# Kernel optimization log

Measured on AMD Instinct MI355X. Metric: run time of the kernel, lower is better.

## Reference

```python
import jax, jax.numpy as jnp
import numpy as np

B = 8192       # batch
HID = 1024     # hidden_dim
HEADS = 8      # head_count
OBS, ACT, N_AGENTS = 128, 32, 4
ENC_IN = N_AGENTS * OBS + ACT   # 544
DEC_IN = (N_AGENTS - 1) * ACT   # 96


def _linear(key, fan_in, fan_out):
    k1, k2 = jax.random.split(key)
    lim = 1.0 / np.sqrt(fan_in)
    W = jax.random.uniform(k1, (fan_in, fan_out), minval=-lim, maxval=lim, dtype=jnp.float32)
    b = jax.random.uniform(k2, (fan_out,), minval=-lim, maxval=lim, dtype=jnp.float32)
    return W, b


def setup_inputs() -> dict:
    key = jax.random.key(0)
    ks = jax.random.split(key, 10)
    s = jax.random.normal(ks[0], (B, N_AGENTS * OBS), dtype=jnp.float32)
    a = jax.random.normal(ks[1], (B, N_AGENTS * ACT), dtype=jnp.float32)
    W_enc_in, b_enc_in = _linear(ks[2], ENC_IN, HID)   # encoder_input_fc
    W_dec_in, b_dec_in = _linear(ks[3], DEC_IN, HID)   # decoder_input_fc
    W_eh, b_eh = _linear(ks[4], HID, HID)              # fc_encoder_input
    head_ks = jax.random.split(ks[5], HEADS)
    Wb = [_linear(k, HID, HID) for k in head_ks]       # fc_encoder_heads
    W_heads = jnp.stack([w for w, _ in Wb], axis=0)    # [H, HID, HID]
    b_heads = jnp.stack([b for _, b in Wb], axis=0)    # [H, HID]
    W_dh, b_dh = _linear(ks[6], HID, HID)              # fc_decoder_input
    W1, b1 = _linear(ks[7], HID, HID)                  # fc1
    W2, b2 = _linear(ks[8], HID, 1)                    # fc2
    return {"s": s, "a": a,
            "W_enc_in": W_enc_in, "b_enc_in": b_enc_in,
            "W_dec_in": W_dec_in, "b_dec_in": b_dec_in,
            "W_eh": W_eh, "b_eh": b_eh,
            "W_heads": W_heads, "b_heads": b_heads,
            "W_dh": W_dh, "b_dh": b_dh,
            "W1": W1, "b1": b1, "W2": W2, "b2": b2}


def reference(s, a, W_enc_in, b_enc_in, W_dec_in, b_dec_in, W_eh, b_eh,
              W_heads, b_heads, W_dh, b_dh, W1, b1, W2, b2):
    relu = jax.nn.relu
    # agent id = 0: own action is a[:, :ACT], others' actions are a[:, ACT:]
    enc_input = jnp.concatenate([s, a[:, :ACT]], axis=1) @ W_enc_in + b_enc_in   # [B, HID]
    dec_input = a[:, ACT:] @ W_dec_in + b_dec_in                                 # [B, HID]
    # Attention_ATT_2
    encoder_h = relu(enc_input @ W_eh + b_eh)                                    # [B, HID]
    encoder_heads = relu(jnp.einsum('bd,hde->hbe', encoder_h, W_heads)
                         + b_heads[:, None, :])                                  # [H, B, HID]
    decoder_H = relu(dec_input @ W_dh + b_dh)                                    # [B, HID]
    scores = jnp.einsum('hbd,bd->bh', encoder_heads, decoder_H)                  # [B, H]
    attn = jax.nn.softmax(scores, axis=1)                                        # [B, H]
    context = jnp.einsum('hbd,bh->bd', encoder_heads, attn)                      # [B, HID]
    x = relu(context @ W1 + b1)
    q = x @ W2 + b2                                                              # [B, 1]
    return q
```

## Files before the change

kernel.cpp:

```cpp
#include <hip/hip_runtime.h>
#include <hip/hip_bf16.h>
#include <hip/hip_fp16.h>

#define BATCH   8192
#define HID     1024
#define HEADS   8
#define BC      2048

typedef unsigned int  u32;
typedef unsigned short u16;
typedef __attribute__((ext_vector_type(8))) short bf16x8;
typedef __attribute__((ext_vector_type(4))) float f32x4;

__device__ __forceinline__ u32 pack_hi2(u32 u0, u32 u1) {
    return (u0 >> 16) | (u1 & 0xFFFF0000u);
}
__device__ __forceinline__ void split1(float x, u16& h, u16& l) {
    const u32 u = __float_as_uint(x);
    h = (u16)(u >> 16);
    const float r = x - __uint_as_float(u & 0xFFFF0000u);
    l = (u16)(__float_as_uint(r) >> 16);
}
__device__ __forceinline__ void splitA4(float4 v, uint2& hi, uint2& lo) {
    u32 u0 = __float_as_uint(v.x), u1 = __float_as_uint(v.y),
        u2 = __float_as_uint(v.z), u3 = __float_as_uint(v.w);
    float r0 = v.x - __uint_as_float(u0 & 0xFFFF0000u);
    float r1 = v.y - __uint_as_float(u1 & 0xFFFF0000u);
    float r2 = v.z - __uint_as_float(u2 & 0xFFFF0000u);
    float r3 = v.w - __uint_as_float(u3 & 0xFFFF0000u);
    hi.x = pack_hi2(u0, u1);
    hi.y = pack_hi2(u2, u3);
    lo.x = pack_hi2(__float_as_uint(r0), __float_as_uint(r1));
    lo.y = pack_hi2(__float_as_uint(r2), __float_as_uint(r3));
}

__device__ __forceinline__ void gld16(const u16* g, u16* l) {
    __builtin_amdgcn_global_load_lds(
        (const __attribute__((address_space(1))) u32*)g,
        (__attribute__((address_space(3))) u32*)l, 16, 0, 0);
}

struct WSplitArgs {
    const float* src[6];
    u16* hi[6];
    u16* lo[6];
};

__global__ __launch_bounds__(256) void split_weight_all(WSplitArgs args)
{
    const int z = blockIdx.z;
    int which, zz = 0;
    if (z < 3)       { which = z; }
    else if (z < 11) { which = 3; zz = z - 3; }
    else             { which = z - 7; }
    const int KT = (which == 4) ? 17 : (which == 5 ? 3 : 32);
    const int kt = blockIdx.x;
    if (kt >= KT) return;
    const int K = KT * 32;
    const long long zoff = (long long)zz * K * 1024;
    const float* W  = args.src[which] + zoff;
    u16* hi = args.hi[which] + zoff;
    u16* lo = args.lo[which] + zoff;

    const int n0  = blockIdx.y * 128;
    const int tid = threadIdx.x;
    const int k   = tid >> 3;
    const int ng  = (tid & 7) * 16;
    const float* src = W + (long long)(kt * 32 + k) * 1024 + n0 + ng;
    u16* dh = hi + ((long long)kt * 1024 + n0) * 32 + k;
    u16* dl = lo + ((long long)kt * 1024 + n0) * 32 + k;
#pragma unroll
    for (int t = 0; t < 4; t++) {
        const float4 v = *(const float4*)(src + t * 4);
        u16 h0, l0, h1, l1, h2, l2, h3, l3;
        split1(v.x, h0, l0); split1(v.y, h1, l1);
        split1(v.z, h2, l2); split1(v.w, h3, l3);
        const int nb = (ng + t * 4) * 32;
        dh[nb]      = h0; dl[nb]      = l0;
        dh[nb + 32] = h1; dl[nb + 32] = l1;
        dh[nb + 64] = h2; dl[nb + 64] = l2;
        dh[nb + 96] = h3; dl[nb + 96] = l3;
    }
}

#define PIPE_GEOM \
    const int tid  = threadIdx.x; \
    const int lane = tid & 63; \
    const int wv   = tid >> 6; \
    const int wm   = wv >> 1, wn = wv & 1; \
    const int fr   = lane & 15; \
    const int fq   = lane >> 4; \
    const int m0   = blockIdx.y * 256; \
    const int n0   = blockIdx.x * 128; \
    const int lro2 = (lane >> 2) * 32 + (((lane & 3) ^ ((lane >> 3) & 3)) * 8); \
    const int fqx2 = (fq ^ ((fr >> 1) & 3)) * 8; \
    const int wr   = wv * 16;

#define PSTAGE(bi_, t_) { \
    u16* db_ = smem + (bi_) * 12288; \
    const long long ao_ = abase + (long long)(t_) * astep; \
    const long long bo_ = bbase + (long long)(t_) * 32768; \
    gld16(Ahp + ao_ + (long long)wr * 32 + lro2, db_ + wr * 32); \
    gld16(Ahp + ao_ + (long long)(128 + wr) * 32 + lro2, db_ + (128 + wr) * 32); \
    gld16(Bhp + bo_ + (long long)wr * 32 + lro2, db_ + 8192 + wr * 32); }

#define PLO(la_, lb_, t_) { \
    const long long ao_ = abase + (long long)(t_) * astep; \
    const long long bo_ = bbase + (long long)(t_) * 32768; \
    _Pragma("unroll") \
    for (int i_ = 0; i_ < 4; i_++) { \
        la_[i_] = *(const bf16x8*)(Alp + ao_ + (long long)(wm * 64 + i_ * 16 + fr) * 32 + fq * 8); \
        lb_[i_] = *(const bf16x8*)(Blp + bo_ + (long long)(wn * 64 + i_ * 16 + fr) * 32 + fq * 8); } }

#define PFRAGS(bi_) \
    const u16* bufp_ = smem + (bi_) * 12288; \
    bf16x8 ah[4], bh[4]; \
    _Pragma("unroll") \
    for (int i_ = 0; i_ < 4; i_++) \
        ah[i_] = *(const bf16x8*)(bufp_ + (wm * 64 + i_ * 16 + fr) * 32 + fqx2); \
    _Pragma("unroll") \
    for (int j_ = 0; j_ < 4; j_++) \
        bh[j_] = *(const bf16x8*)(bufp_ + 8192 + (wn * 64 + j_ * 16 + fr) * 32 + fqx2);

#define PMFMA(la_, lb_) \
    __builtin_amdgcn_sched_barrier(0); \
    __builtin_amdgcn_s_setprio(1); \
    _Pragma("unroll") \
    for (int i_ = 0; i_ < 4; i_++) \
        _Pragma("unroll") \
        for (int j_ = 0; j_ < 4; j_++) \
            acc[i_][j_] = __builtin_amdgcn_mfma_f32_16x16x32_bf16(ah[i_], bh[j_], acc[i_][j_], 0, 0, 0); \
    _Pragma("unroll") \
    for (int i_ = 0; i_ < 4; i_++) \
        _Pragma("unroll") \
        for (int j_ = 0; j_ < 4; j_++) \
            acc[i_][j_] = __builtin_amdgcn_mfma_f32_16x16x32_bf16(ah[i_], lb_[j_], acc[i_][j_], 0, 0, 0); \
    _Pragma("unroll") \
    for (int i_ = 0; i_ < 4; i_++) \
        _Pragma("unroll") \
        for (int j_ = 0; j_ < 4; j_++) \
            acc[i_][j_] = __builtin_amdgcn_mfma_f32_16x16x32_bf16(la_[i_], bh[j_], acc[i_][j_], 0, 0, 0); \
    __builtin_amdgcn_s_setprio(0);

#define PBAR(W_) \
    asm volatile("s_waitcnt vmcnt(" #W_ ")" ::: "memory"); \
    __builtin_amdgcn_s_barrier(); \
    __builtin_amdgcn_sched_barrier(0);

#define PIPE_LOOP \
    const int KT = K >> 5; \
    const long long astep = (long long)MA * 32; \
    const long long abase = ((long long)moff + m0) * 32; \
    const long long bbase = (long long)n0 * 32; \
    bf16x8 loAa[4], loAb[4], loBa[4], loBb[4]; \
    PSTAGE(0, 0); \
    PSTAGE(1, 1); \
    PLO(loAa, loAb, 0); \
    PBAR(11) \
    int be = 0, bo = 1, bs = 2; \
    for (int t = 0; t + 2 < KT; t += 2) { \
        { PFRAGS(be) PSTAGE(bs, t + 2); PLO(loBa, loBb, t + 1); \
          PMFMA(loAa, loAb) PBAR(11) } \
        { PFRAGS(bo) PSTAGE(be, t + 3); PLO(loAa, loAb, t + 2); \
          PMFMA(loBa, loBb) PBAR(11) } \
        const int nb_ = bs; bs = bo; bo = be; be = nb_; \
    } \
    { PFRAGS(be) PLO(loBa, loBb, KT - 1); PMFMA(loAa, loAb) PBAR(8) } \
    { PFRAGS(bo) PMFMA(loBa, loBb) }

template <int RELU, int OUTP>
__global__ __launch_bounds__(512, 2) void gemm_fast(
    const u16* __restrict__ Ahp, const u16* __restrict__ Alp, int MA, int moff,
    const u16* __restrict__ Bhp, const u16* __restrict__ Blp,
    const float* __restrict__ bias,
    float* __restrict__ Cf,
    u16* __restrict__ Chp, u16* __restrict__ Clp, int MC,
    int K)
{
    __shared__ alignas(16) u16 smem[3 * 12288];
    PIPE_GEOM

    f32x4 acc[4][4];
#pragma unroll
    for (int i = 0; i < 4; i++)
#pragma unroll
        for (int j = 0; j < 4; j++) acc[i][j] = 0;

    PIPE_LOOP

#pragma unroll
    for (int j = 0; j < 4; j++) {
        const int n = n0 + wn * 64 + j * 16 + fr;
        const float bb = bias[n];
#pragma unroll
        for (int i = 0; i < 4; i++) {
#pragma unroll
            for (int r = 0; r < 4; r++) {
                const int m = m0 + wm * 64 + i * 16 + fq * 4 + r;
                float v = acc[i][j][r] + bb;
                if (RELU) v = fmaxf(v, 0.0f);
                if (OUTP) {
                    u16 h, l;
                    split1(v, h, l);
                    const long long d = ((long long)(n >> 5) * MC + moff + m) * 32 + (n & 31);
                    Chp[d] = h;
                    Clp[d] = l;
                } else {
                    Cf[(long long)m * 1024 + n] = v;
                }
            }
        }
    }
}

__global__ __launch_bounds__(512, 2) void heads_kernel(
    const u16* __restrict__ Ahp, const u16* __restrict__ Alp, int MA, int moff,
    const u16* __restrict__ Whp, const u16* __restrict__ Wlp,
    const float* __restrict__ b_heads,
    const float* __restrict__ decH,
    __half* __restrict__ headsb,
    float* __restrict__ scoresp)
{
    __shared__ alignas(16) u16 smem[3 * 12288];
    __shared__ float scred[2][256];
    PIPE_GEOM
    const int h = blockIdx.z;
    const u16* Bhp = Whp + (long long)h * 1048576;
    const u16* Blp = Wlp + (long long)h * 1048576;
    const float* bias = b_heads + h * 1024;
    const int K = 1024;

    f32x4 acc[4][4];
#pragma unroll
    for (int i = 0; i < 4; i++)
#pragma unroll
        for (int j = 0; j < 4; j++) acc[i][j] = 0;

    PIPE_LOOP

    float part[4][4];
#pragma unroll
    for (int i = 0; i < 4; i++)
#pragma unroll
        for (int r = 0; r < 4; r++) part[i][r] = 0.0f;

#pragma unroll
    for (int j = 0; j < 4; j++) {
        const int n = n0 + wn * 64 + j * 16 + fr;
        const float bb = bias[n];
#pragma unroll
        for (int i = 0; i < 4; i++) {
#pragma unroll
            for (int r = 0; r < 4; r++) {
                const int b_loc = m0 + wm * 64 + i * 16 + fq * 4 + r;
                const float v = fmaxf(acc[i][j][r] + bb, 0.0f);
                headsb[((long long)b_loc * HEADS + h) * 1024 + n] = __float2half(v);
                part[i][r] = fmaf(v, decH[(long long)b_loc * 1024 + n], part[i][r]);
            }
        }
    }
#pragma unroll
    for (int off = 1; off < 16; off <<= 1)
#pragma unroll
        for (int i = 0; i < 4; i++)
#pragma unroll
            for (int r = 0; r < 4; r++)
                part[i][r] += __shfl_xor(part[i][r], off, 64);

    if (fr == 0) {
#pragma unroll
        for (int i = 0; i < 4; i++)
#pragma unroll
            for (int r = 0; r < 4; r++)
                scred[wn][wm * 64 + i * 16 + fq * 4 + r] = part[i][r];
    }
    __syncthreads();
    if (tid < 256) {
        const float sv = scred[0][tid] + scred[1][tid];
        scoresp[(long long)(h * 8 + blockIdx.x) * BC + m0 + tid] = sv;
    }
}

template <int RELU>
__global__ __launch_bounds__(256) void gemm_cvt(
    const float* __restrict__ src1, int lda1, int kofs1,
    const float* __restrict__ src2, int lda2, int ksplit,
    const u16* __restrict__ Bhp, const u16* __restrict__ Blp,
    const float* __restrict__ bias,
    u16* __restrict__ Chp, u16* __restrict__ Clp, int MC,
    int K)
{
    __shared__ alignas(16) u16 Ah[4096], Al[4096], Bh[4096], Bl[4096];
    const int tid  = threadIdx.x;
    const int lane = tid & 63;
    const int wv   = tid >> 6;
    const int wm   = wv >> 1, wn = wv & 1;
    const int fr   = lane & 15;
    const int fq   = lane >> 4;
    const int m0   = blockIdx.y * 128;
    const int n0   = blockIdx.x * 128;
    const int fqx  = (fq ^ (fr & 3)) * 8;
    const int lro  = (lane >> 2) * 32 + (((lane & 3) ^ ((lane >> 2) & 3)) * 8);
    const int br0  = wv * 16;
    const int br1  = 64 + wv * 16;
    const int ar   = tid >> 3;
    const int akq  = tid & 7;
    const int awoff = (((akq >> 1) ^ (ar & 3)) * 8) + (akq & 1) * 4;

    f32x4 acc[4][4];
#pragma unroll
    for (int i = 0; i < 4; i++)
#pragma unroll
        for (int j = 0; j < 4; j++) acc[i][j] = 0;

    const int KT = K >> 5;
    for (int kt = 0; kt < KT; kt++) {
        const int k0 = kt * 32;
        const float* srcp; int ldk, kc;
        if (k0 < ksplit) { srcp = src1; ldk = lda1; kc = k0 + kofs1; }
        else             { srcp = src2; ldk = lda2; kc = k0 - ksplit; }

        const u16* Bg  = Bhp + ((long long)kt * 1024 + n0) * 32;
        const u16* Bg2 = Blp + ((long long)kt * 1024 + n0) * 32;
        gld16(Bg  + br0 * 32 + lro, &Bh[br0 * 32]);
        gld16(Bg  + br1 * 32 + lro, &Bh[br1 * 32]);
        gld16(Bg2 + br0 * 32 + lro, &Bl[br0 * 32]);
        gld16(Bg2 + br1 * 32 + lro, &Bl[br1 * 32]);

#pragma unroll
        for (int it = 0; it < 4; it++) {
            const int row = ar + it * 32;
            const float4 v = *(const float4*)(srcp + (long long)(m0 + row) * ldk + kc + akq * 4);
            uint2 hi, lo;
            splitA4(v, hi, lo);
            *(uint2*)&Ah[row * 32 + awoff] = hi;
            *(uint2*)&Al[row * 32 + awoff] = lo;
        }
        __syncthreads();

        bf16x8 ah[4], al[4], bh[4], bl[4];
#pragma unroll
        for (int i = 0; i < 4; i++) {
            const int off = (wm * 64 + i * 16 + fr) * 32 + fqx;
            ah[i] = *(const bf16x8*)&Ah[off];
            al[i] = *(const bf16x8*)&Al[off];
        }
#pragma unroll
        for (int j = 0; j < 4; j++) {
            const int off = (wn * 64 + j * 16 + fr) * 32 + fqx;
            bh[j] = *(const bf16x8*)&Bh[off];
            bl[j] = *(const bf16x8*)&Bl[off];
        }
#pragma unroll
        for (int i = 0; i < 4; i++)
#pragma unroll
            for (int j = 0; j < 4; j++) {
                acc[i][j] = __builtin_amdgcn_mfma_f32_16x16x32_bf16(ah[i], bh[j], acc[i][j], 0, 0, 0);
                acc[i][j] = __builtin_amdgcn_mfma_f32_16x16x32_bf16(ah[i], bl[j], acc[i][j], 0, 0, 0);
                acc[i][j] = __builtin_amdgcn_mfma_f32_16x16x32_bf16(al[i], bh[j], acc[i][j], 0, 0, 0);
            }
        __syncthreads();
    }

#pragma unroll
    for (int j = 0; j < 4; j++) {
        const int n = n0 + wn * 64 + j * 16 + fr;
        const float bb = bias[n];
#pragma unroll
        for (int i = 0; i < 4; i++) {
#pragma unroll
            for (int r = 0; r < 4; r++) {
                const int m = m0 + wm * 64 + i * 16 + fq * 4 + r;
                float v = acc[i][j][r] + bb;
                if (RELU) v = fmaxf(v, 0.0f);
                u16 h, l;
                split1(v, h, l);
                const long long d = ((long long)(n >> 5) * MC + m) * 32 + (n & 31);
                Chp[d] = h;
                Clp[d] = l;
            }
        }
    }
}

__global__ __launch_bounds__(256) void context_kernel(
    const __half* __restrict__ headsb, const float* __restrict__ scoresp,
    u16* __restrict__ ctx_hi, u16* __restrict__ ctx_lo, int MC, int row0)
{
    __shared__ float sc_s[64];
    __shared__ float attn_s[HEADS];
    const int b = blockIdx.x;
    const int tid = threadIdx.x;
    if (tid < 64) sc_s[tid] = scoresp[(long long)tid * BC + b];
    __syncthreads();
    if (tid == 0) {
        float sc[HEADS];
#pragma unroll
        for (int h = 0; h < HEADS; h++) {
            float s = 0.0f;
#pragma unroll
            for (int nt = 0; nt < 8; nt++) s += sc_s[h * 8 + nt];
            sc[h] = s;
        }
        float mx = sc[0];
#pragma unroll
        for (int h = 1; h < HEADS; h++) mx = fmaxf(mx, sc[h]);
        float e[HEADS], sum = 0.0f;
#pragma unroll
        for (int h = 0; h < HEADS; h++) { e[h] = __expf(sc[h] - mx); sum += e[h]; }
        const float inv = 1.0f / sum;
#pragma unroll
        for (int h = 0; h < HEADS; h++) attn_s[h] = e[h] * inv;
    }
    __syncthreads();

    const int d = tid * 4;
    float w[HEADS];
#pragma unroll
    for (int h = 0; h < HEADS; h++) w[h] = attn_s[h];
    float4 acc = make_float4(0.f, 0.f, 0.f, 0.f);
#pragma unroll
    for (int h = 0; h < HEADS; h++) {
        const __half2* hp = (const __half2*)(headsb + ((long long)b * HEADS + h) * 1024 + d);
        const float2 f0 = __half22float2(hp[0]);
        const float2 f1 = __half22float2(hp[1]);
        acc.x = fmaf(w[h], f0.x, acc.x);
        acc.y = fmaf(w[h], f0.y, acc.y);
        acc.z = fmaf(w[h], f1.x, acc.z);
        acc.w = fmaf(w[h], f1.y, acc.w);
    }
    uint2 hi, lo;
    splitA4(acc, hi, lo);
    const long long off = ((long long)(d >> 5) * MC + row0 + b) * 32 + (d & 31);
    *(uint2*)(ctx_hi + off) = hi;
    *(uint2*)(ctx_lo + off) = lo;
}

__global__ __launch_bounds__(256) void fc2_kernel(
    const float* __restrict__ x, const float* __restrict__ W2,
    const float* __restrict__ b2, float* __restrict__ q)
{
    const int b   = blockIdx.x;
    const int tid = threadIdx.x;
    __shared__ float red[4];

    const float4 xv = *(const float4*)(x + (long long)b * 1024 + tid * 4);
    const float4 wv = *(const float4*)(W2 + tid * 4);
    float p = xv.x * wv.x + xv.y * wv.y + xv.z * wv.z + xv.w * wv.w;
#pragma unroll
    for (int off = 32; off > 0; off >>= 1) p += __shfl_down(p, off, 64);
    if ((tid & 63) == 0) red[tid >> 6] = p;
    __syncthreads();
    if (tid == 0) q[b] = red[0] + red[1] + red[2] + red[3] + b2[0];
}

extern "C" void kernel_launch(void* const* d_in, const int* in_sizes, int n_in,
                              void* d_out, int out_size, void* d_ws, size_t ws_size,
                              hipStream_t stream)
{
    const float* s        = (const float*)d_in[0];
    const float* a        = (const float*)d_in[1];
    const float* W_enc_in = (const float*)d_in[2];
    const float* b_enc_in = (const float*)d_in[3];
    const float* W_dec_in = (const float*)d_in[4];
    const float* b_dec_in = (const float*)d_in[5];
    const float* W_eh     = (const float*)d_in[6];
    const float* b_eh     = (const float*)d_in[7];
    const float* W_heads  = (const float*)d_in[8];
    const float* b_heads  = (const float*)d_in[9];
    const float* W_dh     = (const float*)d_in[10];
    const float* b_dh     = (const float*)d_in[11];
    const float* W1       = (const float*)d_in[12];
    const float* b1       = (const float*)d_in[13];
    const float* W2       = (const float*)d_in[14];
    const float* b2       = (const float*)d_in[15];
    float* q_out = (float*)d_out;

    u16* P = (u16*)d_ws;
    u16* enc_hi = P; P += 557056;
    u16* enc_lo = P; P += 557056;
    u16* dec_hi = P; P += 98304;
    u16* dec_lo = P; P += 98304;
    u16* eh_hi  = P; P += 1048576;
    u16* eh_lo  = P; P += 1048576;
    u16* dh_hi  = P; P += 1048576;
    u16* dh_lo  = P; P += 1048576;
    u16* w1_hi  = P; P += 1048576;
    u16* w1_lo  = P; P += 1048576;
    u16* wh_hi  = P; P += 8388608;
    u16* wh_lo  = P; P += 8388608;
    char* act = (char*)P;

    const dim3 blk(256);
    const dim3 blk512(512);

    WSplitArgs wa;
    wa.src[0] = W_eh;    wa.hi[0] = eh_hi;  wa.lo[0] = eh_lo;
    wa.src[1] = W_dh;    wa.hi[1] = dh_hi;  wa.lo[1] = dh_lo;
    wa.src[2] = W1;      wa.hi[2] = w1_hi;  wa.lo[2] = w1_lo;
    wa.src[3] = W_heads; wa.hi[3] = wh_hi;  wa.lo[3] = wh_lo;
    wa.src[4] = W_enc_in; wa.hi[4] = enc_hi; wa.lo[4] = enc_lo;
    wa.src[5] = W_dec_in; wa.hi[5] = dec_hi; wa.lo[5] = dec_lo;
    split_weight_all<<<dim3(32, 8, 13), blk, 0, stream>>>(wa);

    const bool high = (ws_size >= 150011904ULL);

    if (high) {
        u16*    bufA_hi = (u16*)act;
        u16*    bufA_lo = bufA_hi + 8388608;
        __half* headsb  = (__half*)act;
        u16*    encH_hi = (u16*)(act + 33554432);
        u16*    encH_lo = encH_hi + 8388608;
        float*  decH    = (float*)(act + 2LL * 33554432);
        float*  scoresp = (float*)(act + 3LL * 33554432);

        const dim3 ggc(8, 64, 1);
        const dim3 ggf(8, 32, 1);
        gemm_cvt<0><<<ggc, blk, 0, stream>>>(s, 512, 0, a, 128, 512,
            enc_hi, enc_lo, b_enc_in, bufA_hi, bufA_lo, 8192, 544);
        gemm_fast<1, 1><<<ggf, blk512, 0, stream>>>(bufA_hi, bufA_lo, 8192, 0,
            eh_hi, eh_lo, b_eh, nullptr, encH_hi, encH_lo, 8192, 1024);
        gemm_cvt<0><<<ggc, blk, 0, stream>>>(a, 128, 32, a, 128, 1 << 28,
            dec_hi, dec_lo, b_dec_in, bufA_hi, bufA_lo, 8192, 96);
        gemm_fast<1, 0><<<ggf, blk512, 0, stream>>>(bufA_hi, bufA_lo, 8192, 0,
            dh_hi, dh_lo, b_dh, decH, nullptr, nullptr, 0, 1024);

        for (int c = 0; c < BATCH / BC; c++) {
            heads_kernel<<<dim3(8, BC / 256, 8), blk512, 0, stream>>>(
                encH_hi, encH_lo, 8192, c * BC, wh_hi, wh_lo, b_heads,
                decH + (long long)c * BC * 1024, headsb, scoresp);
            context_kernel<<<dim3(BC), blk, 0, stream>>>(
                headsb, scoresp, encH_hi, encH_lo, 8192, c * BC);
        }
        gemm_fast<1, 0><<<ggf, blk512, 0, stream>>>(encH_hi, encH_lo, 8192, 0,
            w1_hi, w1_lo, b1, decH, nullptr, nullptr, 0, 1024);
        fc2_kernel<<<dim3(BATCH), blk, 0, stream>>>(decH, W2, b2, q_out);
    } else {
        __half* headsb  = (__half*)act;
        u16*    bufA_hi = (u16*)act;
        u16*    bufA_lo = bufA_hi + 2097152;
        u16*    encH_hi = (u16*)(act + 33554432);
        u16*    encH_lo = encH_hi + 2097152;
        float*  decH    = (float*)(act + 33554432 + 8388608);
        float*  scoresp = (float*)(act + 33554432 + 2LL * 8388608);

        const dim3 ggc(8, BC / 128, 1);
        const dim3 ggf(8, BC / 256, 1);
        for (int c = 0; c < BATCH / BC; c++) {
            const float* sC = s + (long long)c * BC * 512;
            const float* aC = a + (long long)c * BC * 128;
            gemm_cvt<0><<<ggc, blk, 0, stream>>>(sC, 512, 0, aC, 128, 512,
                enc_hi, enc_lo, b_enc_in, bufA_hi, bufA_lo, BC, 544);
            gemm_fast<1, 1><<<ggf, blk512, 0, stream>>>(bufA_hi, bufA_lo, BC, 0,
                eh_hi, eh_lo, b_eh, nullptr, encH_hi, encH_lo, BC, 1024);
            gemm_cvt<0><<<ggc, blk, 0, stream>>>(aC, 128, 32, aC, 128, 1 << 28,
                dec_hi, dec_lo, b_dec_in, bufA_hi, bufA_lo, BC, 96);
            gemm_fast<1, 0><<<ggf, blk512, 0, stream>>>(bufA_hi, bufA_lo, BC, 0,
                dh_hi, dh_lo, b_dh, decH, nullptr, nullptr, 0, 1024);
            heads_kernel<<<dim3(8, BC / 256, 8), blk512, 0, stream>>>(
                encH_hi, encH_lo, BC, 0, wh_hi, wh_lo, b_heads,
                decH, headsb, scoresp);
            context_kernel<<<dim3(BC), blk, 0, stream>>>(
                headsb, scoresp, encH_hi, encH_lo, BC, 0);
            gemm_fast<1, 0><<<ggf, blk512, 0, stream>>>(encH_hi, encH_lo, BC, 0,
                w1_hi, w1_lo, b1, decH, nullptr, nullptr, 0, 1024);
            fc2_kernel<<<dim3(BC), blk, 0, stream>>>(decH, W2, b2, q_out + (long long)c * BC);
        }
    }
}
```

Baseline: 808.5 us.

## Stage lo-split operands through LDS and enlarge heads GEMM tile to 256x256

The GEMM pipelines now stage both the hi and lo bf16 split operands through LDS instead of reading the lo parts straight from global memory into registers. The inner loop is reorganised into half-tile MFMA quarters separated by barriers. The heads kernel moves to a 256x256 tile with double buffering and 8 waves laid out 2x4, which halves the N-blocks and the score partials the context kernel must sum. This aims to cut redundant global reads and raise reuse per block. In exchange it uses much more LDS, more accumulator registers (acc[8][4] under launch_bounds 512,2) and more barriers, which could lower occupancy or cause spills.

```diff
diff --git a/kernel.cpp b/kernel.cpp
--- a/kernel.cpp
+++ b/kernel.cpp
@@ -83,7 +83,30 @@
     }
 }
 
-#define PIPE_GEOM \
+#define MFMA_Q(IB, JB) \
+    __builtin_amdgcn_s_setprio(1); \
+    _Pragma("unroll") \
+    for (int i_ = 0; i_ < 4; i_++) \
+        _Pragma("unroll") \
+        for (int j_ = 0; j_ < 2; j_++) \
+            acc[(IB) + i_][(JB) + j_] = __builtin_amdgcn_mfma_f32_16x16x32_bf16(ah[i_], bh[(JB) + j_], acc[(IB) + i_][(JB) + j_], 0, 0, 0); \
+    _Pragma("unroll") \
+    for (int i_ = 0; i_ < 4; i_++) \
+        _Pragma("unroll") \
+        for (int j_ = 0; j_ < 2; j_++) \
+            acc[(IB) + i_][(JB) + j_] = __builtin_amdgcn_mfma_f32_16x16x32_bf16(ah[i_], bl[(JB) + j_], acc[(IB) + i_][(JB) + j_], 0, 0, 0); \
+    _Pragma("unroll") \
+    for (int i_ = 0; i_ < 4; i_++) \
+        _Pragma("unroll") \
+        for (int j_ = 0; j_ < 2; j_++) \
+            acc[(IB) + i_][(JB) + j_] = __builtin_amdgcn_mfma_f32_16x16x32_bf16(al[i_], bh[(JB) + j_], acc[(IB) + i_][(JB) + j_], 0, 0, 0); \
+    __builtin_amdgcn_s_setprio(0);
+
+#define SBAR() \
+    __builtin_amdgcn_s_barrier(); \
+    __builtin_amdgcn_sched_barrier(0);
+
+#define G_GEOM \
     const int tid  = threadIdx.x; \
     const int lane = tid & 63; \
     const int wv   = tid >> 6; \
@@ -94,79 +117,65 @@
     const int n0   = blockIdx.x * 128; \
     const int lro2 = (lane >> 2) * 32 + (((lane & 3) ^ ((lane >> 3) & 3)) * 8); \
     const int fqx2 = (fq ^ ((fr >> 1) & 3)) * 8; \
-    const int wr   = wv * 16;
-
-#define PSTAGE(bi_, t_) { \
-    u16* db_ = smem + (bi_) * 12288; \
+    const int wrA  = wv * 32; \
+    const int wrB  = wv * 16;
+
+#define G_STAGE_A(buf_, t_) { \
+    u16* d_ = (buf_); \
     const long long ao_ = abase + (long long)(t_) * astep; \
+    gld16(Ahp + ao_ + (long long)wrA * 32 + lro2, d_ + wrA * 32); \
+    gld16(Ahp + ao_ + (long long)(wrA + 16) * 32 + lro2, d_ + (wrA + 16) * 32); \
+    gld16(Alp + ao_ + (long long)wrA * 32 + lro2, d_ + 8192 + wrA * 32); \
+    gld16(Alp + ao_ + (long long)(wrA + 16) * 32 + lro2, d_ + 8192 + (wrA + 16) * 32); }
+
+#define G_STAGE_B(buf_, t_) { \
+    u16* d_ = (buf_); \
     const long long bo_ = bbase + (long long)(t_) * 32768; \
-    gld16(Ahp + ao_ + (long long)wr * 32 + lro2, db_ + wr * 32); \
-    gld16(Ahp + ao_ + (long long)(128 + wr) * 32 + lro2, db_ + (128 + wr) * 32); \
-    gld16(Bhp + bo_ + (long long)wr * 32 + lro2, db_ + 8192 + wr * 32); }
-
-#define PLO(la_, lb_, t_) { \
-    const long long ao_ = abase + (long long)(t_) * astep; \
-    const long long bo_ = bbase + (long long)(t_) * 32768; \
+    gld16(Bhp + bo_ + (long long)wrB * 32 + lro2, d_ + 16384 + wrB * 32); \
+    gld16(Blp + bo_ + (long long)wrB * 32 + lro2, d_ + 20480 + wrB * 32); }
+
+#define G_RD_A(bp_) \
     _Pragma("unroll") \
     for (int i_ = 0; i_ < 4; i_++) { \
-        la_[i_] = *(const bf16x8*)(Alp + ao_ + (long long)(wm * 64 + i_ * 16 + fr) * 32 + fq * 8); \
-        lb_[i_] = *(const bf16x8*)(Blp + bo_ + (long long)(wn * 64 + i_ * 16 + fr) * 32 + fq * 8); } }
-
-#define PFRAGS(bi_) \
-    const u16* bufp_ = smem + (bi_) * 12288; \
-    bf16x8 ah[4], bh[4]; \
+        const int off_ = (wm * 64 + i_ * 16 + fr) * 32 + fqx2; \
+        ah[i_] = *(const bf16x8*)((bp_) + off_); \
+        al[i_] = *(const bf16x8*)((bp_) + 8192 + off_); }
+
+#define G_RD_B(bp_, JB) \
     _Pragma("unroll") \
-    for (int i_ = 0; i_ < 4; i_++) \
-        ah[i_] = *(const bf16x8*)(bufp_ + (wm * 64 + i_ * 16 + fr) * 32 + fqx2); \
-    _Pragma("unroll") \
-    for (int j_ = 0; j_ < 4; j_++) \
-        bh[j_] = *(const bf16x8*)(bufp_ + 8192 + (wn * 64 + j_ * 16 + fr) * 32 + fqx2);
-
-#define PMFMA(la_, lb_) \
-    __builtin_amdgcn_sched_barrier(0); \
-    __builtin_amdgcn_s_setprio(1); \
-    _Pragma("unroll") \
-    for (int i_ = 0; i_ < 4; i_++) \
-        _Pragma("unroll") \
-        for (int j_ = 0; j_ < 4; j_++) \
-            acc[i_][j_] = __builtin_amdgcn_mfma_f32_16x16x32_bf16(ah[i_], bh[j_], acc[i_][j_], 0, 0, 0); \
-    _Pragma("unroll") \
-    for (int i_ = 0; i_ < 4; i_++) \
-        _Pragma("unroll") \
-        for (int j_ = 0; j_ < 4; j_++) \
-            acc[i_][j_] = __builtin_amdgcn_mfma_f32_16x16x32_bf16(ah[i_], lb_[j_], acc[i_][j_], 0, 0, 0); \
-    _Pragma("unroll") \
-    for (int i_ = 0; i_ < 4; i_++) \
-        _Pragma("unroll") \
-        for (int j_ = 0; j_ < 4; j_++) \
-            acc[i_][j_] = __builtin_amdgcn_mfma_f32_16x16x32_bf16(la_[i_], bh[j_], acc[i_][j_], 0, 0, 0); \
-    __builtin_amdgcn_s_setprio(0);
-
-#define PBAR(W_) \
-    asm volatile("s_waitcnt vmcnt(" #W_ ")" ::: "memory"); \
-    __builtin_amdgcn_s_barrier(); \
-    __builtin_amdgcn_sched_barrier(0);
-
-#define PIPE_LOOP \
+    for (int j_ = 0; j_ < 2; j_++) { \
+        const int off_ = (wn * 64 + ((JB) + j_) * 16 + fr) * 32 + fqx2; \
+        bh[(JB) + j_] = *(const bf16x8*)((bp_) + 16384 + off_); \
+        bl[(JB) + j_] = *(const bf16x8*)((bp_) + 20480 + off_); }
+
+#define G_LOOP \
     const int KT = K >> 5; \
     const long long astep = (long long)MA * 32; \
     const long long abase = ((long long)moff + m0) * 32; \
     const long long bbase = (long long)n0 * 32; \
-    bf16x8 loAa[4], loAb[4], loBa[4], loBb[4]; \
-    PSTAGE(0, 0); \
-    PSTAGE(1, 1); \
-    PLO(loAa, loAb, 0); \
-    PBAR(11) \
-    int be = 0, bo = 1, bs = 2; \
-    for (int t = 0; t + 2 < KT; t += 2) { \
-        { PFRAGS(be) PSTAGE(bs, t + 2); PLO(loBa, loBb, t + 1); \
-          PMFMA(loAa, loAb) PBAR(11) } \
-        { PFRAGS(bo) PSTAGE(be, t + 3); PLO(loAa, loAb, t + 2); \
-          PMFMA(loBa, loBb) PBAR(11) } \
-        const int nb_ = bs; bs = bo; bo = be; be = nb_; \
-    } \
-    { PFRAGS(be) PLO(loBa, loBb, KT - 1); PMFMA(loAa, loAb) PBAR(8) } \
-    { PFRAGS(bo) PMFMA(loBa, loBb) }
+    G_STAGE_A(smem, 0); G_STAGE_B(smem, 0); \
+    G_STAGE_A(smem + 24576, 1); G_STAGE_B(smem + 24576, 1); \
+    asm volatile("s_waitcnt vmcnt(6)" ::: "memory"); \
+    SBAR() \
+    for (int t = 0; t < KT; t++) { \
+        const u16* bp = smem + (t % 3) * 24576; \
+        u16* nb = smem + ((t + 2) % 3) * 24576; \
+        const bool more = (t + 2 < KT); \
+        bf16x8 ah[4], al[4], bh[4], bl[4]; \
+        G_RD_A(bp) \
+        G_RD_B(bp, 0) \
+        if (more) G_STAGE_A(nb, t + 2); \
+        __builtin_amdgcn_sched_barrier(0); \
+        MFMA_Q(0, 0) \
+        SBAR() \
+        G_RD_B(bp, 2) \
+        if (more) G_STAGE_B(nb, t + 2); \
+        __builtin_amdgcn_sched_barrier(0); \
+        MFMA_Q(0, 2) \
+        if (more) { asm volatile("s_waitcnt vmcnt(6)" ::: "memory"); } \
+        else      { asm volatile("s_waitcnt vmcnt(0)" ::: "memory"); } \
+        SBAR() \
+    }
 
 template <int RELU, int OUTP>
 __global__ __launch_bounds__(512, 2) void gemm_fast(
@@ -177,8 +186,8 @@
     u16* __restrict__ Chp, u16* __restrict__ Clp, int MC,
     int K)
 {
-    __shared__ alignas(16) u16 smem[3 * 12288];
-    PIPE_GEOM
+    __shared__ alignas(16) u16 smem[3 * 24576];
+    G_GEOM
 
     f32x4 acc[4][4];
 #pragma unroll
@@ -186,7 +195,7 @@
 #pragma unroll
         for (int j = 0; j < 4; j++) acc[i][j] = 0;
 
-    PIPE_LOOP
+    G_LOOP
 
 #pragma unroll
     for (int j = 0; j < 4; j++) {
@@ -213,6 +222,36 @@
     }
 }
 
+#define H_STAGE_A(buf_, t_) { \
+    u16* d_ = (buf_); \
+    const long long ao_ = abase + (long long)(t_) * astep; \
+    gld16(Ahp + ao_ + (long long)wrA * 32 + lro2, d_ + wrA * 32); \
+    gld16(Ahp + ao_ + (long long)(wrA + 16) * 32 + lro2, d_ + (wrA + 16) * 32); \
+    gld16(Alp + ao_ + (long long)wrA * 32 + lro2, d_ + 8192 + wrA * 32); \
+    gld16(Alp + ao_ + (long long)(wrA + 16) * 32 + lro2, d_ + 8192 + (wrA + 16) * 32); }
+
+#define H_STAGE_B(buf_, t_) { \
+    u16* d_ = (buf_); \
+    const long long bo_ = bbase + (long long)(t_) * 32768; \
+    gld16(Bhp + bo_ + (long long)wrA * 32 + lro2, d_ + 16384 + wrA * 32); \
+    gld16(Bhp + bo_ + (long long)(wrA + 16) * 32 + lro2, d_ + 16384 + (wrA + 16) * 32); \
+    gld16(Blp + bo_ + (long long)wrA * 32 + lro2, d_ + 24576 + wrA * 32); \
+    gld16(Blp + bo_ + (long long)(wrA + 16) * 32 + lro2, d_ + 24576 + (wrA + 16) * 32); }
+
+#define H_RD_A(bp_, RB) \
+    _Pragma("unroll") \
+    for (int i_ = 0; i_ < 4; i_++) { \
+        const int off_ = ((RB) + i_ * 16 + fr) * 32 + fqx2; \
+        ah[i_] = *(const bf16x8*)((bp_) + off_); \
+        al[i_] = *(const bf16x8*)((bp_) + 8192 + off_); }
+
+#define H_RD_B(bp_, JB) \
+    _Pragma("unroll") \
+    for (int j_ = 0; j_ < 2; j_++) { \
+        const int off_ = (wn * 64 + ((JB) + j_) * 16 + fr) * 32 + fqx2; \
+        bh[(JB) + j_] = *(const bf16x8*)((bp_) + 16384 + off_); \
+        bl[(JB) + j_] = *(const bf16x8*)((bp_) + 24576 + off_); }
+
 __global__ __launch_bounds__(512, 2) void heads_kernel(
     const u16* __restrict__ Ahp, const u16* __restrict__ Alp, int MA, int moff,
     const u16* __restrict__ Whp, const u16* __restrict__ Wlp,
@@ -221,26 +260,68 @@
     __half* __restrict__ headsb,
     float* __restrict__ scoresp)
 {
-    __shared__ alignas(16) u16 smem[3 * 12288];
-    __shared__ float scred[2][256];
-    PIPE_GEOM
+    __shared__ alignas(16) u16 smem[2 * 32768];
+    __shared__ float scred[4][256];
+    const int tid  = threadIdx.x;
+    const int lane = tid & 63;
+    const int wv   = tid >> 6;
+    const int wm   = wv >> 2;
+    const int wn   = wv & 3;
+    const int fr   = lane & 15;
+    const int fq   = lane >> 4;
+    const int m0   = blockIdx.y * 256;
+    const int n0   = blockIdx.x * 256;
+    const int lro2 = (lane >> 2) * 32 + (((lane & 3) ^ ((lane >> 3) & 3)) * 8);
+    const int fqx2 = (fq ^ ((fr >> 1) & 3)) * 8;
+    const int wrA  = wv * 32;
     const int h = blockIdx.z;
     const u16* Bhp = Whp + (long long)h * 1048576;
     const u16* Blp = Wlp + (long long)h * 1048576;
     const float* bias = b_heads + h * 1024;
-    const int K = 1024;
-
-    f32x4 acc[4][4];
-#pragma unroll
-    for (int i = 0; i < 4; i++)
+
+    f32x4 acc[8][4];
+#pragma unroll
+    for (int i = 0; i < 8; i++)
 #pragma unroll
         for (int j = 0; j < 4; j++) acc[i][j] = 0;
 
-    PIPE_LOOP
-
-    float part[4][4];
-#pragma unroll
-    for (int i = 0; i < 4; i++)
+    const long long astep = (long long)MA * 32;
+    const long long abase = ((long long)moff + m0) * 32;
+    const long long bbase = (long long)n0 * 32;
+
+    H_STAGE_A(smem, 0);
+    H_STAGE_B(smem, 0);
+    asm volatile("s_waitcnt vmcnt(0)" ::: "memory");
+    SBAR()
+
+    for (int t = 0; t < 32; t++) {
+        const u16* bp = smem + (t & 1) * 32768;
+        u16* nb = smem + ((t + 1) & 1) * 32768;
+        const bool more = (t + 1 < 32);
+        bf16x8 ah[4], al[4], bh[4], bl[4];
+        H_RD_A(bp, wm * 128)
+        H_RD_B(bp, 0)
+        if (more) H_STAGE_A(nb, t + 1);
+        __builtin_amdgcn_sched_barrier(0);
+        MFMA_Q(0, 0)
+        SBAR()
+        H_RD_B(bp, 2)
+        if (more) H_STAGE_B(nb, t + 1);
+        __builtin_amdgcn_sched_barrier(0);
+        MFMA_Q(0, 2)
+        SBAR()
+        H_RD_A(bp, wm * 128 + 64)
+        __builtin_amdgcn_sched_barrier(0);
+        MFMA_Q(4, 0)
+        SBAR()
+        MFMA_Q(4, 2)
+        asm volatile("s_waitcnt vmcnt(0)" ::: "memory");
+        SBAR()
+    }
+
+    float part[8][4];
+#pragma unroll
+    for (int i = 0; i < 8; i++)
 #pragma unroll
         for (int r = 0; r < 4; r++) part[i][r] = 0.0f;
 
@@ -249,10 +330,10 @@
         const int n = n0 + wn * 64 + j * 16 + fr;
         const float bb = bias[n];
 #pragma unroll
-        for (int i = 0; i < 4; i++) {
+        for (int i = 0; i < 8; i++) {
 #pragma unroll
             for (int r = 0; r < 4; r++) {
-                const int b_loc = m0 + wm * 64 + i * 16 + fq * 4 + r;
+                const int b_loc = m0 + wm * 128 + i * 16 + fq * 4 + r;
                 const float v = fmaxf(acc[i][j][r] + bb, 0.0f);
                 headsb[((long long)b_loc * HEADS + h) * 1024 + n] = __float2half(v);
                 part[i][r] = fmaf(v, decH[(long long)b_loc * 1024 + n], part[i][r]);
@@ -262,22 +343,22 @@
 #pragma unroll
     for (int off = 1; off < 16; off <<= 1)
 #pragma unroll
-        for (int i = 0; i < 4; i++)
+        for (int i = 0; i < 8; i++)
 #pragma unroll
             for (int r = 0; r < 4; r++)
                 part[i][r] += __shfl_xor(part[i][r], off, 64);
 
     if (fr == 0) {
 #pragma unroll
-        for (int i = 0; i < 4; i++)
+        for (int i = 0; i < 8; i++)
 #pragma unroll
             for (int r = 0; r < 4; r++)
-                scred[wn][wm * 64 + i * 16 + fq * 4 + r] = part[i][r];
+                scred[wn][wm * 128 + i * 16 + fq * 4 + r] = part[i][r];
     }
     __syncthreads();
     if (tid < 256) {
-        const float sv = scred[0][tid] + scred[1][tid];
-        scoresp[(long long)(h * 8 + blockIdx.x) * BC + m0 + tid] = sv;
+        const float sv = scred[0][tid] + scred[1][tid] + scred[2][tid] + scred[3][tid];
+        scoresp[(long long)(h * 4 + blockIdx.x) * BC + m0 + tid] = sv;
     }
 }
 
@@ -387,11 +468,11 @@
     const __half* __restrict__ headsb, const float* __restrict__ scoresp,
     u16* __restrict__ ctx_hi, u16* __restrict__ ctx_lo, int MC, int row0)
 {
-    __shared__ float sc_s[64];
+    __shared__ float sc_s[32];
     __shared__ float attn_s[HEADS];
     const int b = blockIdx.x;
     const int tid = threadIdx.x;
-    if (tid < 64) sc_s[tid] = scoresp[(long long)tid * BC + b];
+    if (tid < 32) sc_s[tid] = scoresp[(long long)tid * BC + b];
     __syncthreads();
     if (tid == 0) {
         float sc[HEADS];
@@ -399,7 +480,7 @@
         for (int h = 0; h < HEADS; h++) {
             float s = 0.0f;
 #pragma unroll
-            for (int nt = 0; nt < 8; nt++) s += sc_s[h * 8 + nt];
+            for (int nt = 0; nt < 4; nt++) s += sc_s[h * 4 + nt];
             sc[h] = s;
         }
         float mx = sc[0];
@@ -526,7 +607,7 @@
             dh_hi, dh_lo, b_dh, decH, nullptr, nullptr, 0, 1024);
 
         for (int c = 0; c < BATCH / BC; c++) {
-            heads_kernel<<<dim3(8, BC / 256, 8), blk512, 0, stream>>>(
+            heads_kernel<<<dim3(4, BC / 256, 8), blk512, 0, stream>>>(
                 encH_hi, encH_lo, 8192, c * BC, wh_hi, wh_lo, b_heads,
                 decH + (long long)c * BC * 1024, headsb, scoresp);
             context_kernel<<<dim3(BC), blk, 0, stream>>>(
@@ -557,7 +638,7 @@
                 dec_hi, dec_lo, b_dec_in, bufA_hi, bufA_lo, BC, 96);
             gemm_fast<1, 0><<<ggf, blk512, 0, stream>>>(bufA_hi, bufA_lo, BC, 0,
                 dh_hi, dh_lo, b_dh, decH, nullptr, nullptr, 0, 1024);
-            heads_kernel<<<dim3(8, BC / 256, 8), blk512, 0, stream>>>(
+            heads_kernel<<<dim3(4, BC / 256, 8), blk512, 0, stream>>>(
                 encH_hi, encH_lo, BC, 0, wh_hi, wh_lo, b_heads,
                 decH, headsb, scoresp);
             context_kernel<<<dim3(BC), blk, 0, stream>>>(
```

New measurement: 751.3 us. -7.1%, faster.
